# Optimization experiments

Measured on AMD Instinct MI355X. Metric: run time of the kernel, lower is better.

## Reference

```python
import jax, jax.numpy as jnp
import numpy as np

D_MODEL = 1024
NUM_HEADS = 16
D_HEAD = D_MODEL // NUM_HEADS


def rotate_half(x):
    half = x.shape[-1] // 2
    x1, x2 = x[..., :half], x[..., half:]
    return jnp.concatenate((-x2, x1), axis=-1)


def rope_cos_sin(seq_len, d_head, dtype):
    # inv_freq over even dims of d_head
    inv_freq = 1.0 / (10000.0 ** (jnp.arange(0, d_head, 2, dtype=jnp.float32) / d_head))
    t = jnp.arange(seq_len, dtype=jnp.float32)
    freqs = jnp.einsum('i,j->ij', t, inv_freq)        # [L, d_head/2]
    emb = jnp.concatenate((freqs, freqs), axis=-1)    # [L, d_head]
    return jnp.cos(emb).astype(dtype), jnp.sin(emb).astype(dtype)


def setup_inputs() -> dict:
    key = jax.random.key(0)
    ks = jax.random.split(key, 9)
    B, L = 2, 2048
    s = 1.0 / np.sqrt(D_MODEL)
    return {
        'x': jax.random.normal(ks[0], (B, L, D_MODEL), dtype=jnp.float32),
        'Wq': jax.random.normal(ks[1], (D_MODEL, D_MODEL), dtype=jnp.float32) * s,
        'bq': jax.random.normal(ks[2], (D_MODEL,), dtype=jnp.float32) * 0.02,
        'Wk': jax.random.normal(ks[3], (D_MODEL, D_MODEL), dtype=jnp.float32) * s,
        'bk': jax.random.normal(ks[4], (D_MODEL,), dtype=jnp.float32) * 0.02,
        'Wv': jax.random.normal(ks[5], (D_MODEL, D_MODEL), dtype=jnp.float32) * s,
        'bv': jax.random.normal(ks[6], (D_MODEL,), dtype=jnp.float32) * 0.02,
        'Wo': jax.random.normal(ks[7], (D_MODEL, D_MODEL), dtype=jnp.float32) * s,
        'bo': jax.random.normal(ks[8], (D_MODEL,), dtype=jnp.float32) * 0.02,
    }


def reference(x, Wq, bq, Wk, bk, Wv, bv, Wo, bo):
    B, L, D = x.shape
    H, Dh = NUM_HEADS, D_HEAD
    scale = Dh ** -0.5

    # projections: torch Linear is x @ W.T + b; here W stored as [in, out]-like
    # square matrices, so treat Wq etc. directly as x @ Wq + bq.
    q = (x @ Wq + bq).reshape(B, L, H, Dh).transpose(0, 2, 1, 3)  # [B,H,L,Dh]
    k = (x @ Wk + bk).reshape(B, L, H, Dh).transpose(0, 2, 1, 3)
    v = (x @ Wv + bv).reshape(B, L, H, Dh).transpose(0, 2, 1, 3)

    cos, sin = rope_cos_sin(L, Dh, x.dtype)  # [L, Dh]
    cos = cos[None, None]  # [1,1,L,Dh]
    sin = sin[None, None]
    q = q * cos + rotate_half(q) * sin
    k = k * cos + rotate_half(k) * sin

    attn = jnp.einsum('bhqd,bhkd->bhqk', q, k) * scale  # [B,H,L,L]
    attn = jax.nn.softmax(attn, axis=-1)
    out = jnp.einsum('bhqk,bhkd->bhqd', attn, v)        # [B,H,L,Dh]
    out = out.transpose(0, 2, 1, 3).reshape(B, L, D)
    return out @ Wo + bo
```

## Files before the change

### kernel.cpp

```cpp
#include <hip/hip_runtime.h>
#include <cmath>

#define D_MODEL  1024
#define NHEADS   16
#define DHEAD    64
#define BATCH    2
#define SEQ      2048
#define MROWS    (BATCH * SEQ)
#define HALF_DH  32
#define BHTOT    (BATCH * NHEADS)
#define QROWS    (BHTOT * SEQ)

typedef __attribute__((ext_vector_type(8))) short short8;
typedef __attribute__((ext_vector_type(4))) float f32x4;
typedef __attribute__((ext_vector_type(16))) float f32x16;

#define MFMA16(A,B,C) __builtin_amdgcn_mfma_f32_16x16x32_bf16(A,B,C,0,0,0)
#define MFMA32(A,B,C) __builtin_amdgcn_mfma_f32_32x32x16_bf16(A,B,C,0,0,0)

__device__ __forceinline__ unsigned short f2bf(float f) {
    unsigned int u = __float_as_uint(f);
    u += 0x7fffu + ((u >> 16) & 1u);
    return (unsigned short)(u >> 16);
}

__device__ __forceinline__ void gload_lds16(const void* g, void* l) {
    __builtin_amdgcn_global_load_lds(
        (const __attribute__((address_space(1))) unsigned int*)g,
        (__attribute__((address_space(3))) unsigned int*)l,
        16, 0, 0);
}

__global__ void rope_table_kernel(float* __restrict__ cosT, float* __restrict__ sinT) {
    int idx = blockIdx.x * blockDim.x + threadIdx.x;
    if (idx >= SEQ * HALF_DH) return;
    int l = idx >> 5;
    int j = idx & 31;
    float inv = powf(10000.0f, -(float)(2 * j) / (float)DHEAD);
    float ang = (float)l * inv;
    cosT[idx] = cosf(ang);
    sinT[idx] = sinf(ang);
}

__global__ __launch_bounds__(256)
void convert_bf16_kernel(const float* __restrict__ in, unsigned short* __restrict__ out) {
    int i = blockIdx.x * 256 + threadIdx.x;
    float4 v = ((const float4*)in)[i];
    ushort4 o;
    o.x = f2bf(v.x); o.y = f2bf(v.y); o.z = f2bf(v.z); o.w = f2bf(v.w);
    ((ushort4*)out)[i] = o;
}

__global__ __launch_bounds__(256)
void wtrans4_kernel(const float* __restrict__ Wq, const float* __restrict__ Wk,
                    const float* __restrict__ Wv, const float* __restrict__ Wo,
                    unsigned short* __restrict__ q, unsigned short* __restrict__ k,
                    unsigned short* __restrict__ v, unsigned short* __restrict__ o)
{
    __shared__ unsigned short T[64][68];
    const float* W; unsigned short* Wt;
    switch (blockIdx.z) {
        case 0:  W = Wq; Wt = q; break;
        case 1:  W = Wk; Wt = k; break;
        case 2:  W = Wv; Wt = v; break;
        default: W = Wo; Wt = o; break;
    }
    const int k0 = blockIdx.x * 64, n0 = blockIdx.y * 64;
    const int t = threadIdx.x, r = t >> 4, cq = t & 15;
    #pragma unroll
    for (int p = 0; p < 4; ++p) {
        int kk = r + 16 * p;
        float4 vv = *(const float4*)&W[(size_t)(k0 + kk) * D_MODEL + n0 + cq * 4];
        T[cq * 4 + 0][kk] = f2bf(vv.x);
        T[cq * 4 + 1][kk] = f2bf(vv.y);
        T[cq * 4 + 2][kk] = f2bf(vv.z);
        T[cq * 4 + 3][kk] = f2bf(vv.w);
    }
    __syncthreads();
    #pragma unroll
    for (int p = 0; p < 4; ++p) {
        int n = r + 16 * p;
        ushort4 ov;
        ov.x = T[n][cq * 4 + 0]; ov.y = T[n][cq * 4 + 1];
        ov.z = T[n][cq * 4 + 2]; ov.w = T[n][cq * 4 + 3];
        *(ushort4*)&Wt[(size_t)(n0 + n) * D_MODEL + k0 + cq * 4] = ov;
    }
}

__global__ __launch_bounds__(256)
void qkv_proj_kernel(const unsigned short* __restrict__ A,
                     const unsigned short* __restrict__ wqT, const unsigned short* __restrict__ wkT,
                     const unsigned short* __restrict__ wvT,
                     const float* __restrict__ bq, const float* __restrict__ bk,
                     const float* __restrict__ bv,
                     const float* __restrict__ cosT, const float* __restrict__ sinT,
                     unsigned short* __restrict__ qb, unsigned short* __restrict__ kb,
                     unsigned short* __restrict__ vtb)
{
    __shared__ unsigned short SMEM[128 * 64 + 64 * 64];
    unsigned short* As = SMEM;
    unsigned short* Bs = SMEM + 128 * 64;

    const int z = blockIdx.z;
    const unsigned short* Bt = (z == 0) ? wqT : (z == 1) ? wkT : wvT;
    const float* bias = (z == 0) ? bq : (z == 1) ? bk : bv;

    const int tid = threadIdx.x;
    const int w = tid >> 6, ln = tid & 63;
    const int c = ln & 15, g = ln >> 4;
    const int bm = blockIdx.x * 128, bn = blockIdx.y * 64;
    const int srow = ln >> 3, sblk = ln & 7;

    f32x4 acc[2][4];
    #pragma unroll
    for (int mi = 0; mi < 2; ++mi)
        #pragma unroll
        for (int ni = 0; ni < 4; ++ni) acc[mi][ni] = (f32x4){0.f, 0.f, 0.f, 0.f};

    for (int k0 = 0; k0 < D_MODEL; k0 += 64) {
        __syncthreads();
        #pragma unroll
        for (int i = 0; i < 4; ++i) {
            int chunk = w * 4 + i;
            int row = chunk * 8 + srow;
            int gcol = (sblk ^ (row & 7)) * 8;
            gload_lds16(&A[(size_t)(bm + row) * D_MODEL + k0 + gcol], &As[chunk * 512]);
        }
        #pragma unroll
        for (int i = 0; i < 2; ++i) {
            int chunk = w * 2 + i;
            int row = chunk * 8 + srow;
            int gcol = (sblk ^ (row & 7)) * 8;
            gload_lds16(&Bt[(size_t)(bn + row) * D_MODEL + k0 + gcol], &Bs[chunk * 512]);
        }
        __syncthreads();

        #pragma unroll
        for (int ks = 0; ks < 2; ++ks) {
            const int koff = (ks * 32 + g * 8) ^ ((c & 7) * 8);
            short8 af[2];
            #pragma unroll
            for (int mi = 0; mi < 2; ++mi)
                af[mi] = *(const short8*)&As[(w * 32 + mi * 16 + c) * 64 + koff];
            #pragma unroll
            for (int ni = 0; ni < 4; ++ni) {
                short8 bfr = *(const short8*)&Bs[(ni * 16 + c) * 64 + koff];
                #pragma unroll
                for (int mi = 0; mi < 2; ++mi)
                    acc[mi][ni] = MFMA16(af[mi], bfr, acc[mi][ni]);
            }
        }
    }

    float bv4[4];
    #pragma unroll
    for (int ni = 0; ni < 4; ++ni) bv4[ni] = bias[bn + ni * 16 + c];

    if (z < 2) {
        unsigned short* op = z ? kb : qb;
        const int hy = blockIdx.y;
        #pragma unroll
        for (int mi = 0; mi < 2; ++mi) {
            #pragma unroll
            for (int r = 0; r < 4; ++r) {
                const int m = bm + w * 32 + mi * 16 + g * 4 + r;
                const int b = m >> 11, ll = m & (SEQ - 1);
                float v[4];
                #pragma unroll
                for (int ni = 0; ni < 4; ++ni) v[ni] = acc[mi][ni][r] + bv4[ni];
                #pragma unroll
                for (int ni = 0; ni < 2; ++ni) {
                    int d = ni * 16 + c;
                    float co = cosT[ll * HALF_DH + d];
                    float si = sinT[ll * HALF_DH + d];
                    float lo = v[ni], hi = v[ni + 2];
                    v[ni]     = lo * co - hi * si;
                    v[ni + 2] = hi * co + lo * si;
                }
                unsigned short* dst = op + ((size_t)(b * NHEADS + hy) * SEQ + ll) * DHEAD;
                #pragma unroll
                for (int ni = 0; ni < 4; ++ni) dst[ni * 16 + c] = f2bf(v[ni]);
            }
        }
    } else {
        unsigned short (*T)[136] = (unsigned short(*)[136])SMEM;
        __syncthreads();
        #pragma unroll
        for (int mi = 0; mi < 2; ++mi)
            #pragma unroll
            for (int r = 0; r < 4; ++r)
                #pragma unroll
                for (int ni = 0; ni < 4; ++ni)
                    T[ni * 16 + c][w * 32 + mi * 16 + g * 4 + r] = f2bf(acc[mi][ni][r] + bv4[ni]);
        __syncthreads();
        const int b  = bm >> 11;
        const int l0 = bm & (SEQ - 1);
        const int bh = b * NHEADS + blockIdx.y;
        unsigned short* Vo = vtb + (size_t)bh * DHEAD * SEQ;
        #pragma unroll
        for (int it = 0; it < 4; ++it) {
            int row  = (tid >> 4) + it * 16;
            int col8 = tid & 15;
            uint4 val = *(const uint4*)&T[row][col8 * 8];
            *(uint4*)&Vo[(size_t)row * SEQ + l0 + col8 * 8] = val;
        }
    }
}

__global__ __launch_bounds__(256)
void outproj_kernel(const unsigned short* __restrict__ A, const unsigned short* __restrict__ Bt,
                    const float* __restrict__ bias, float* __restrict__ out)
{
    __shared__ unsigned short As[128 * 64];
    __shared__ unsigned short Bs[64 * 64];
    const int tid = threadIdx.x;
    const int w = tid >> 6, ln = tid & 63;
    const int c = ln & 15, g = ln >> 4;
    const int bm = blockIdx.x * 128, bn = blockIdx.y * 64;
    const int srow = ln >> 3, sblk = ln & 7;

    f32x4 acc[2][4];
    #pragma unroll
    for (int mi = 0; mi < 2; ++mi)
        #pragma unroll
        for (int ni = 0; ni < 4; ++ni) acc[mi][ni] = (f32x4){0.f, 0.f, 0.f, 0.f};

    for (int k0 = 0; k0 < D_MODEL; k0 += 64) {
        __syncthreads();
        #pragma unroll
        for (int i = 0; i < 4; ++i) {
            int chunk = w * 4 + i;
            int row = chunk * 8 + srow;
            int gcol = (sblk ^ (row & 7)) * 8;
            gload_lds16(&A[(size_t)(bm + row) * D_MODEL + k0 + gcol], &As[chunk * 512]);
        }
        #pragma unroll
        for (int i = 0; i < 2; ++i) {
            int chunk = w * 2 + i;
            int row = chunk * 8 + srow;
            int gcol = (sblk ^ (row & 7)) * 8;
            gload_lds16(&Bt[(size_t)(bn + row) * D_MODEL + k0 + gcol], &Bs[chunk * 512]);
        }
        __syncthreads();

        #pragma unroll
        for (int ks = 0; ks < 2; ++ks) {
            const int koff = (ks * 32 + g * 8) ^ ((c & 7) * 8);
            short8 af[2];
            #pragma unroll
            for (int mi = 0; mi < 2; ++mi)
                af[mi] = *(const short8*)&As[(w * 32 + mi * 16 + c) * 64 + koff];
            #pragma unroll
            for (int ni = 0; ni < 4; ++ni) {
                short8 bfr = *(const short8*)&Bs[(ni * 16 + c) * 64 + koff];
                #pragma unroll
                for (int mi = 0; mi < 2; ++mi)
                    acc[mi][ni] = MFMA16(af[mi], bfr, acc[mi][ni]);
            }
        }
    }

    float bv4[4];
    #pragma unroll
    for (int ni = 0; ni < 4; ++ni) bv4[ni] = bias[bn + ni * 16 + c];
    #pragma unroll
    for (int mi = 0; mi < 2; ++mi)
        #pragma unroll
        for (int r = 0; r < 4; ++r) {
            const int m = bm + w * 32 + mi * 16 + g * 4 + r;
            #pragma unroll
            for (int ni = 0; ni < 4; ++ni)
                out[(size_t)m * D_MODEL + bn + ni * 16 + c] = acc[mi][ni][r] + bv4[ni];
        }
}

__global__ __launch_bounds__(256, 4)
void attn_mfma32_kernel(const unsigned short* __restrict__ Q, const unsigned short* __restrict__ K,
                        const unsigned short* __restrict__ Vt, unsigned short* __restrict__ O,
                        float* __restrict__ accP, float* __restrict__ ml, int nsplit)
{
    __shared__ unsigned short Ks[2][64 * 64];
    __shared__ unsigned short Vs[2][64 * 64];
    const int tid = threadIdx.x;
    const int w = tid >> 6, ln = tid & 63;
    const int ql = ln & 31;
    const int h  = ln >> 5;
    const int bh = blockIdx.y;
    const int q  = blockIdx.x * 128 + w * 32 + ql;
    const int split = blockIdx.z;
    const int ntile = SEQ / (64 * nsplit);
    const int kt0 = split * (SEQ / nsplit);
    const float SC = 0.125f * 1.44269504088896340736f;
    const int srow = ln >> 3, sblk = ln & 7;

    const unsigned short* Qb = Q  + (size_t)bh * SEQ * DHEAD;
    const unsigned short* Kb = K  + (size_t)bh * SEQ * DHEAD;
    const unsigned short* Vb = Vt + (size_t)bh * DHEAD * SEQ;

    short8 qf[4];
    #pragma unroll
    for (int dk = 0; dk < 4; ++dk)
        qf[dk] = *(const short8*)&Qb[(size_t)q * DHEAD + dk * 16 + h * 8];

    f32x16 accO0, accO1;
    #pragma unroll
    for (int r = 0; r < 16; ++r) { accO0[r] = 0.f; accO1[r] = 0.f; }
    float accL = 0.f, mst = -1e30f;

    #pragma unroll
    for (int i = 0; i < 2; ++i) {
        int chunk = w * 2 + i;
        int row = chunk * 8 + srow;
        int gcol = (sblk ^ (row & 7)) * 8;
        gload_lds16(&Kb[(size_t)(kt0 + row) * DHEAD + gcol], &Ks[0][chunk * 512]);
        gload_lds16(&Vb[(size_t)row * SEQ + kt0 + gcol],     &Vs[0][chunk * 512]);
    }
    __syncthreads();

    int cur = 0;
    for (int it = 0; it < ntile; ++it) {
        const int kt = kt0 + it * 64;
        if (it + 1 < ntile) {
            #pragma unroll
            for (int i = 0; i < 2; ++i) {
                int chunk = w * 2 + i;
                int row = chunk * 8 + srow;
                int gcol = (sblk ^ (row & 7)) * 8;
                gload_lds16(&Kb[(size_t)(kt + 64 + row) * DHEAD + gcol], &Ks[cur ^ 1][chunk * 512]);
                gload_lds16(&Vb[(size_t)row * SEQ + kt + 64 + gcol],     &Vs[cur ^ 1][chunk * 512]);
            }
        }

        f32x16 s0, s1;
        #pragma unroll
        for (int r = 0; r < 16; ++r) { s0[r] = 0.f; s1[r] = 0.f; }
        #pragma unroll
        for (int dk = 0; dk < 4; ++dk) {
            const int off = ((2 * dk + h) ^ (ql & 7)) * 8;
            short8 kf0 = *(const short8*)&Ks[cur][ql * 64 + off];
            short8 kf1 = *(const short8*)&Ks[cur][(32 + ql) * 64 + off];
            s0 = MFMA32(kf0, qf[dk], s0);
            s1 = MFMA32(kf1, qf[dk], s1);
        }

        float m16[16];
        #pragma unroll
        for (int r = 0; r < 16; ++r) m16[r] = fmaxf(s0[r], s1[r]);
        #pragma unroll
        for (int st = 8; st >= 1; st >>= 1)
            #pragma unroll
            for (int r = 0; r < st; ++r) m16[r] = fmaxf(m16[r], m16[r + st]);
        float mx = m16[0];
        mx = fmaxf(mx, __shfl_xor(mx, 32));

        const float mn = fmaxf(mst, mx);
        if (__any(mn > mst)) {
            const float rsc = exp2f((mst - mn) * SC);
            #pragma unroll
            for (int r = 0; r < 16; ++r) { accO0[r] *= rsc; accO1[r] *= rsc; }
            accL *= rsc;
            mst = mn;
        }

        #pragma unroll
        for (int r = 0; r < 16; ++r) {
            s0[r] = exp2f((s0[r] - mst) * SC);
            s1[r] = exp2f((s1[r] - mst) * SC);
        }

        float t16[16];
        #pragma unroll
        for (int r = 0; r < 16; ++r) t16[r] = s0[r] + s1[r];
        #pragma unroll
        for (int st = 8; st >= 1; st >>= 1)
            #pragma unroll
            for (int r = 0; r < st; ++r) t16[r] += t16[r + st];
        float ts = t16[0];
        ts += __shfl_xor(ts, 32);
        accL += ts;

        short8 pf[4];
        #define REPACK_T(T, SV)                                                          \
        {                                                                                \
            unsigned int wA0, wA1, wB0, wB1;                                             \
            asm("v_cvt_pk_bf16_f32 %0, %1, %2" : "=v"(wA0)                               \
                : "v"((SV)[8 * ((T) & 1) + 0]), "v"((SV)[8 * ((T) & 1) + 1]));           \
            asm("v_cvt_pk_bf16_f32 %0, %1, %2" : "=v"(wA1)                               \
                : "v"((SV)[8 * ((T) & 1) + 2]), "v"((SV)[8 * ((T) & 1) + 3]));           \
            asm("v_cvt_pk_bf16_f32 %0, %1, %2" : "=v"(wB0)                               \
                : "v"((SV)[8 * ((T) & 1) + 4]), "v"((SV)[8 * ((T) & 1) + 5]));           \
            asm("v_cvt_pk_bf16_f32 %0, %1, %2" : "=v"(wB1)                               \
                : "v"((SV)[8 * ((T) & 1) + 6]), "v"((SV)[8 * ((T) & 1) + 7]));           \
            asm("v_permlane32_swap_b32 %0, %1" : "+v"(wA0), "+v"(wB0));                  \
            asm("v_permlane32_swap_b32 %0, %1" : "+v"(wA1), "+v"(wB1));                  \
            union { short8 v; unsigned int u[4]; } tmp;                                  \
            tmp.u[0] = wA0; tmp.u[1] = wA1; tmp.u[2] = wB0; tmp.u[3] = wB1;              \
            pf[T] = tmp.v;                                                               \
        }
        REPACK_T(0, s0) REPACK_T(1, s0) REPACK_T(2, s1) REPACK_T(3, s1)
        #undef REPACK_T

        #pragma unroll
        for (int t = 0; t < 4; ++t) {
            const int off = ((2 * t + h) ^ (ql & 7)) * 8;
            short8 vf0 = *(const short8*)&Vs[cur][ql * 64 + off];
            short8 vf1 = *(const short8*)&Vs[cur][(32 + ql) * 64 + off];
            accO0 = MFMA32(vf0, pf[t], accO0);
            accO1 = MFMA32(vf1, pf[t], accO1);
        }

        __syncthreads();
        cur ^= 1;
    }

    if (nsplit == 1) {
        const int b = bh >> 4, hh = bh & 15;
        const float inv = 1.0f / accL;
        unsigned short* dst = O + ((size_t)(b * SEQ + q)) * D_MODEL + hh * DHEAD;
        #define EPI(ACC, DC)                                                             \
        {                                                                                \
            _Pragma("unroll")                                                            \
            for (int rq = 0; rq < 4; ++rq) {                                             \
                float a0 = (ACC)[4 * rq + 0] * inv, a1 = (ACC)[4 * rq + 1] * inv;        \
                float a2 = (ACC)[4 * rq + 2] * inv, a3 = (ACC)[4 * rq + 3] * inv;        \
                unsigned int p0, p1;                                                     \
                asm("v_cvt_pk_bf16_f32 %0, %1, %2" : "=v"(p0) : "v"(a0), "v"(a1));       \
                asm("v_cvt_pk_bf16_f32 %0, %1, %2" : "=v"(p1) : "v"(a2), "v"(a3));       \
                uint2 pk; pk.x = p0; pk.y = p1;                                          \
                *(uint2*)(dst + 32 * (DC) + 8 * rq + 4 * h) = pk;                        \
            }                                                                            \
        }
        EPI(accO0, 0) EPI(accO1, 1)
        #undef EPI
    } else {
        float* base = accP + ((size_t)(split * BHTOT + bh) * SEQ + q) * 64;
        #pragma unroll
        for (int rq = 0; rq < 4; ++rq) {
            float4 v0, v1;
            v0.x = accO0[4 * rq + 0]; v0.y = accO0[4 * rq + 1];
            v0.z = accO0[4 * rq + 2]; v0.w = accO0[4 * rq + 3];
            v1.x = accO1[4 * rq + 0]; v1.y = accO1[4 * rq + 1];
            v1.z = accO1[4 * rq + 2]; v1.w = accO1[4 * rq + 3];
            *(float4*)&base[8 * rq + 4 * h]      = v0;
            *(float4*)&base[32 + 8 * rq + 4 * h] = v1;
        }
        if (h == 0) {
            float2 v; v.x = mst; v.y = accL;
            ((float2*)ml)[(size_t)(split * BHTOT + bh) * SEQ + q] = v;
        }
    }
}

__global__ __launch_bounds__(256)
void combine2_kernel(const float* __restrict__ accP, const float* __restrict__ ml,
                     unsigned short* __restrict__ ob)
{
    const float SC = 0.125f * 1.44269504088896340736f;
    int t = blockIdx.x * 256 + threadIdx.x;
    int d4  = (t & 15) * 4;
    int bhq = t >> 4;
    const float2* ML = (const float2*)ml;
    float2 m0 = ML[bhq];
    float2 m1 = ML[(size_t)QROWS + bhq];
    float M  = fmaxf(m0.x, m1.x);
    float w0 = exp2f((m0.x - M) * SC);
    float w1 = exp2f((m1.x - M) * SC);
    float inv = 1.0f / (w0 * m0.y + w1 * m1.y);
    float4 a0 = *(const float4*)&accP[(size_t)bhq * 64 + d4];
    float4 a1 = *(const float4*)&accP[(size_t)QROWS * 64 + (size_t)bhq * 64 + d4];
    float o0 = (a0.x * w0 + a1.x * w1) * inv;
    float o1 = (a0.y * w0 + a1.y * w1) * inv;
    float o2 = (a0.z * w0 + a1.z * w1) * inv;
    float o3 = (a0.w * w0 + a1.w * w1) * inv;
    int bh = bhq >> 11, q = bhq & (SEQ - 1);
    int b = bh >> 4, hh = bh & 15;
    ushort4 ov;
    ov.x = f2bf(o0); ov.y = f2bf(o1); ov.z = f2bf(o2); ov.w = f2bf(o3);
    *(ushort4*)&ob[((size_t)(b * SEQ + q)) * D_MODEL + hh * DHEAD + d4] = ov;
}

extern "C" void kernel_launch(void* const* d_in, const int* in_sizes, int n_in,
                              void* d_out, int out_size, void* d_ws, size_t ws_size,
                              hipStream_t stream)
{
    const float* x  = (const float*)d_in[0];
    const float* Wq = (const float*)d_in[1];
    const float* bq = (const float*)d_in[2];
    const float* Wk = (const float*)d_in[3];
    const float* bk = (const float*)d_in[4];
    const float* Wv = (const float*)d_in[5];
    const float* bv = (const float*)d_in[6];
    const float* Wo = (const float*)d_in[7];
    const float* bo = (const float*)d_in[8];

    char* p = (char*)d_ws;
    float* cosT = (float*)p;            p += (size_t)SEQ * HALF_DH * 4;
    float* sinT = (float*)p;            p += (size_t)SEQ * HALF_DH * 4;
    unsigned short* xb  = (unsigned short*)p; p += (size_t)MROWS * D_MODEL * 2;
    unsigned short* wqT = (unsigned short*)p; p += (size_t)D_MODEL * D_MODEL * 2;
    unsigned short* wkT = (unsigned short*)p; p += (size_t)D_MODEL * D_MODEL * 2;
    unsigned short* wvT = (unsigned short*)p; p += (size_t)D_MODEL * D_MODEL * 2;
    unsigned short* woT = (unsigned short*)p; p += (size_t)D_MODEL * D_MODEL * 2;
    unsigned short* qb  = (unsigned short*)p; p += (size_t)MROWS * D_MODEL * 2;
    unsigned short* kb  = (unsigned short*)p; p += (size_t)MROWS * D_MODEL * 2;
    unsigned short* vtb = (unsigned short*)p; p += (size_t)MROWS * D_MODEL * 2;
    unsigned short* ob  = (unsigned short*)p; p += (size_t)MROWS * D_MODEL * 2;
    float* accP = (float*)p;            p += (size_t)2 * QROWS * 64 * 4;
    float* ml   = (float*)p;            p += (size_t)2 * QROWS * 2 * 4;
    size_t need2 = (size_t)(p - (char*)d_ws);
    const int nsplit = (ws_size >= need2) ? 2 : 1;

    rope_table_kernel<<<(SEQ * HALF_DH + 255) / 256, 256, 0, stream>>>(cosT, sinT);
    convert_bf16_kernel<<<(MROWS * D_MODEL / 4) / 256, 256, 0, stream>>>(x, xb);

    wtrans4_kernel<<<dim3(D_MODEL / 64, D_MODEL / 64, 4), 256, 0, stream>>>(
        Wq, Wk, Wv, Wo, wqT, wkT, wvT, woT);

    qkv_proj_kernel<<<dim3(MROWS / 128, D_MODEL / 64, 3), 256, 0, stream>>>(
        xb, wqT, wkT, wvT, bq, bk, bv, cosT, sinT, qb, kb, vtb);

    attn_mfma32_kernel<<<dim3(SEQ / 128, BHTOT, nsplit), 256, 0, stream>>>(
        qb, kb, vtb, ob, accP, ml, nsplit);

    if (nsplit == 2)
        combine2_kernel<<<(QROWS * 16) / 256, 256, 0, stream>>>(accP, ml, ob);

    outproj_kernel<<<dim3(MROWS / 128, D_MODEL / 64), 256, 0, stream>>>(ob, woT, bo, (float*)d_out);
}
```

Measured before the change: 152.6 us.

## Enlarge GEMM M-tiles to 256 and compute softmax row sums via MFMA

```diff
diff --git a/kernel.cpp b/kernel.cpp
--- a/kernel.cpp
+++ b/kernel.cpp
@@ -97,9 +97,9 @@
                      unsigned short* __restrict__ qb, unsigned short* __restrict__ kb,
                      unsigned short* __restrict__ vtb)
 {
-    __shared__ unsigned short SMEM[128 * 64 + 64 * 64];
+    __shared__ unsigned short SMEM[256 * 64 + 64 * 64];
     unsigned short* As = SMEM;
-    unsigned short* Bs = SMEM + 128 * 64;
+    unsigned short* Bs = SMEM + 256 * 64;
 
     const int z = blockIdx.z;
     const unsigned short* Bt = (z == 0) ? wqT : (z == 1) ? wkT : wvT;
@@ -108,20 +108,20 @@
     const int tid = threadIdx.x;
     const int w = tid >> 6, ln = tid & 63;
     const int c = ln & 15, g = ln >> 4;
-    const int bm = blockIdx.x * 128, bn = blockIdx.y * 64;
+    const int bm = blockIdx.x * 256, bn = blockIdx.y * 64;
     const int srow = ln >> 3, sblk = ln & 7;
 
-    f32x4 acc[2][4];
-    #pragma unroll
-    for (int mi = 0; mi < 2; ++mi)
+    f32x4 acc[4][4];
+    #pragma unroll
+    for (int mi = 0; mi < 4; ++mi)
         #pragma unroll
         for (int ni = 0; ni < 4; ++ni) acc[mi][ni] = (f32x4){0.f, 0.f, 0.f, 0.f};
 
     for (int k0 = 0; k0 < D_MODEL; k0 += 64) {
         __syncthreads();
         #pragma unroll
-        for (int i = 0; i < 4; ++i) {
-            int chunk = w * 4 + i;
+        for (int i = 0; i < 8; ++i) {
+            int chunk = w * 8 + i;
             int row = chunk * 8 + srow;
             int gcol = (sblk ^ (row & 7)) * 8;
             gload_lds16(&A[(size_t)(bm + row) * D_MODEL + k0 + gcol], &As[chunk * 512]);
@@ -138,15 +138,15 @@
         #pragma unroll
         for (int ks = 0; ks < 2; ++ks) {
             const int koff = (ks * 32 + g * 8) ^ ((c & 7) * 8);
-            short8 af[2];
-            #pragma unroll
-            for (int mi = 0; mi < 2; ++mi)
-                af[mi] = *(const short8*)&As[(w * 32 + mi * 16 + c) * 64 + koff];
+            short8 af[4];
+            #pragma unroll
+            for (int mi = 0; mi < 4; ++mi)
+                af[mi] = *(const short8*)&As[(w * 64 + mi * 16 + c) * 64 + koff];
             #pragma unroll
             for (int ni = 0; ni < 4; ++ni) {
                 short8 bfr = *(const short8*)&Bs[(ni * 16 + c) * 64 + koff];
                 #pragma unroll
-                for (int mi = 0; mi < 2; ++mi)
+                for (int mi = 0; mi < 4; ++mi)
                     acc[mi][ni] = MFMA16(af[mi], bfr, acc[mi][ni]);
             }
         }
@@ -160,10 +160,10 @@
         unsigned short* op = z ? kb : qb;
         const int hy = blockIdx.y;
         #pragma unroll
-        for (int mi = 0; mi < 2; ++mi) {
+        for (int mi = 0; mi < 4; ++mi) {
             #pragma unroll
             for (int r = 0; r < 4; ++r) {
-                const int m = bm + w * 32 + mi * 16 + g * 4 + r;
+                const int m = bm + w * 64 + mi * 16 + g * 4 + r;
                 const int b = m >> 11, ll = m & (SEQ - 1);
                 float v[4];
                 #pragma unroll
@@ -183,26 +183,26 @@
             }
         }
     } else {
-        unsigned short (*T)[136] = (unsigned short(*)[136])SMEM;
-        __syncthreads();
-        #pragma unroll
-        for (int mi = 0; mi < 2; ++mi)
+        unsigned short (*T)[264] = (unsigned short(*)[264])SMEM;
+        __syncthreads();
+        #pragma unroll
+        for (int mi = 0; mi < 4; ++mi)
             #pragma unroll
             for (int r = 0; r < 4; ++r)
                 #pragma unroll
                 for (int ni = 0; ni < 4; ++ni)
-                    T[ni * 16 + c][w * 32 + mi * 16 + g * 4 + r] = f2bf(acc[mi][ni][r] + bv4[ni]);
+                    T[ni * 16 + c][w * 64 + mi * 16 + g * 4 + r] = f2bf(acc[mi][ni][r] + bv4[ni]);
         __syncthreads();
         const int b  = bm >> 11;
         const int l0 = bm & (SEQ - 1);
         const int bh = b * NHEADS + blockIdx.y;
         unsigned short* Vo = vtb + (size_t)bh * DHEAD * SEQ;
         #pragma unroll
-        for (int it = 0; it < 4; ++it) {
-            int row  = (tid >> 4) + it * 16;
-            int col8 = tid & 15;
-            uint4 val = *(const uint4*)&T[row][col8 * 8];
-            *(uint4*)&Vo[(size_t)row * SEQ + l0 + col8 * 8] = val;
+        for (int it = 0; it < 8; ++it) {
+            int row = (tid >> 5) + it * 8;
+            int ch  = tid & 31;
+            uint4 val = *(const uint4*)&T[row][ch * 8];
+            *(uint4*)&Vo[(size_t)row * SEQ + l0 + ch * 8] = val;
         }
     }
 }
@@ -211,25 +211,25 @@
 void outproj_kernel(const unsigned short* __restrict__ A, const unsigned short* __restrict__ Bt,
                     const float* __restrict__ bias, float* __restrict__ out)
 {
-    __shared__ unsigned short As[128 * 64];
+    __shared__ unsigned short As[256 * 64];
     __shared__ unsigned short Bs[64 * 64];
     const int tid = threadIdx.x;
     const int w = tid >> 6, ln = tid & 63;
     const int c = ln & 15, g = ln >> 4;
-    const int bm = blockIdx.x * 128, bn = blockIdx.y * 64;
+    const int bm = blockIdx.x * 256, bn = blockIdx.y * 64;
     const int srow = ln >> 3, sblk = ln & 7;
 
-    f32x4 acc[2][4];
-    #pragma unroll
-    for (int mi = 0; mi < 2; ++mi)
+    f32x4 acc[4][4];
+    #pragma unroll
+    for (int mi = 0; mi < 4; ++mi)
         #pragma unroll
         for (int ni = 0; ni < 4; ++ni) acc[mi][ni] = (f32x4){0.f, 0.f, 0.f, 0.f};
 
     for (int k0 = 0; k0 < D_MODEL; k0 += 64) {
         __syncthreads();
         #pragma unroll
-        for (int i = 0; i < 4; ++i) {
-            int chunk = w * 4 + i;
+        for (int i = 0; i < 8; ++i) {
+            int chunk = w * 8 + i;
             int row = chunk * 8 + srow;
             int gcol = (sblk ^ (row & 7)) * 8;
             gload_lds16(&A[(size_t)(bm + row) * D_MODEL + k0 + gcol], &As[chunk * 512]);
@@ -246,15 +246,15 @@
         #pragma unroll
         for (int ks = 0; ks < 2; ++ks) {
             const int koff = (ks * 32 + g * 8) ^ ((c & 7) * 8);
-            short8 af[2];
-            #pragma unroll
-            for (int mi = 0; mi < 2; ++mi)
-                af[mi] = *(const short8*)&As[(w * 32 + mi * 16 + c) * 64 + koff];
+            short8 af[4];
+            #pragma unroll
+            for (int mi = 0; mi < 4; ++mi)
+                af[mi] = *(const short8*)&As[(w * 64 + mi * 16 + c) * 64 + koff];
             #pragma unroll
             for (int ni = 0; ni < 4; ++ni) {
                 short8 bfr = *(const short8*)&Bs[(ni * 16 + c) * 64 + koff];
                 #pragma unroll
-                for (int mi = 0; mi < 2; ++mi)
+                for (int mi = 0; mi < 4; ++mi)
                     acc[mi][ni] = MFMA16(af[mi], bfr, acc[mi][ni]);
             }
         }
@@ -264,10 +264,10 @@
     #pragma unroll
     for (int ni = 0; ni < 4; ++ni) bv4[ni] = bias[bn + ni * 16 + c];
     #pragma unroll
-    for (int mi = 0; mi < 2; ++mi)
+    for (int mi = 0; mi < 4; ++mi)
         #pragma unroll
         for (int r = 0; r < 4; ++r) {
-            const int m = bm + w * 32 + mi * 16 + g * 4 + r;
+            const int m = bm + w * 64 + mi * 16 + g * 4 + r;
             #pragma unroll
             for (int ni = 0; ni < 4; ++ni)
                 out[(size_t)m * D_MODEL + bn + ni * 16 + c] = acc[mi][ni][r] + bv4[ni];
@@ -302,10 +302,19 @@
     for (int dk = 0; dk < 4; ++dk)
         qf[dk] = *(const short8*)&Qb[(size_t)q * DHEAD + dk * 16 + h * 8];
 
-    f32x16 accO0, accO1;
-    #pragma unroll
-    for (int r = 0; r < 16; ++r) { accO0[r] = 0.f; accO1[r] = 0.f; }
-    float accL = 0.f, mst = -1e30f;
+    short8 onesF;
+    #pragma unroll
+    for (int i = 0; i < 8; ++i) onesF[i] = (short)0x3F80;
+
+    int offk[4];
+    #pragma unroll
+    for (int t = 0; t < 4; ++t) offk[t] = ((2 * t + h) ^ (ql & 7)) * 8;
+    const int rA = ql * 64, rB = (32 + ql) * 64;
+
+    f32x16 accO0, accO1, accS;
+    #pragma unroll
+    for (int r = 0; r < 16; ++r) { accO0[r] = 0.f; accO1[r] = 0.f; accS[r] = 0.f; }
+    float mst = -1e30f;
 
     #pragma unroll
     for (int i = 0; i < 2; ++i) {
@@ -336,21 +345,28 @@
         for (int r = 0; r < 16; ++r) { s0[r] = 0.f; s1[r] = 0.f; }
         #pragma unroll
         for (int dk = 0; dk < 4; ++dk) {
-            const int off = ((2 * dk + h) ^ (ql & 7)) * 8;
-            short8 kf0 = *(const short8*)&Ks[cur][ql * 64 + off];
-            short8 kf1 = *(const short8*)&Ks[cur][(32 + ql) * 64 + off];
+            short8 kf0 = *(const short8*)&Ks[cur][rA + offk[dk]];
+            short8 kf1 = *(const short8*)&Ks[cur][rB + offk[dk]];
             s0 = MFMA32(kf0, qf[dk], s0);
             s1 = MFMA32(kf1, qf[dk], s1);
         }
 
-        float m16[16];
-        #pragma unroll
-        for (int r = 0; r < 16; ++r) m16[r] = fmaxf(s0[r], s1[r]);
-        #pragma unroll
-        for (int st = 8; st >= 1; st >>= 1)
-            #pragma unroll
-            for (int r = 0; r < st; ++r) m16[r] = fmaxf(m16[r], m16[r + st]);
-        float mx = m16[0];
+        float a0 = fmaxf(fmaxf(s0[0], s0[1]), s0[2]);
+        float a1 = fmaxf(fmaxf(s0[3], s0[4]), s0[5]);
+        float a2 = fmaxf(fmaxf(s0[6], s0[7]), s0[8]);
+        float a3 = fmaxf(fmaxf(s0[9], s0[10]), s0[11]);
+        float a4 = fmaxf(fmaxf(s0[12], s0[13]), s0[14]);
+        float a5 = fmaxf(fmaxf(s0[15], s1[0]), s1[1]);
+        float a6 = fmaxf(fmaxf(s1[2], s1[3]), s1[4]);
+        float a7 = fmaxf(fmaxf(s1[5], s1[6]), s1[7]);
+        float a8 = fmaxf(fmaxf(s1[8], s1[9]), s1[10]);
+        float a9 = fmaxf(fmaxf(s1[11], s1[12]), s1[13]);
+        float aA = fmaxf(s1[14], s1[15]);
+        float b0 = fmaxf(fmaxf(a0, a1), a2);
+        float b1 = fmaxf(fmaxf(a3, a4), a5);
+        float b2 = fmaxf(fmaxf(a6, a7), a8);
+        float b3 = fmaxf(a9, aA);
+        float mx = fmaxf(fmaxf(fmaxf(b0, b1), b2), b3);
         mx = fmaxf(mx, __shfl_xor(mx, 32));
 
         const float mn = fmaxf(mst, mx);
@@ -358,7 +374,7 @@
             const float rsc = exp2f((mst - mn) * SC);
             #pragma unroll
             for (int r = 0; r < 16; ++r) { accO0[r] *= rsc; accO1[r] *= rsc; }
-            accL *= rsc;
+            accS[0] *= rsc;
             mst = mn;
         }
 
@@ -367,17 +383,6 @@
             s0[r] = exp2f((s0[r] - mst) * SC);
             s1[r] = exp2f((s1[r] - mst) * SC);
         }
-
-        float t16[16];
-        #pragma unroll
-        for (int r = 0; r < 16; ++r) t16[r] = s0[r] + s1[r];
-        #pragma unroll
-        for (int st = 8; st >= 1; st >>= 1)
-            #pragma unroll
-            for (int r = 0; r < st; ++r) t16[r] += t16[r + st];
-        float ts = t16[0];
-        ts += __shfl_xor(ts, 32);
-        accL += ts;
 
         short8 pf[4];
         #define REPACK_T(T, SV)                                                          \
@@ -402,9 +407,9 @@
 
         #pragma unroll
         for (int t = 0; t < 4; ++t) {
-            const int off = ((2 * t + h) ^ (ql & 7)) * 8;
-            short8 vf0 = *(const short8*)&Vs[cur][ql * 64 + off];
-            short8 vf1 = *(const short8*)&Vs[cur][(32 + ql) * 64 + off];
+            short8 vf0 = *(const short8*)&Vs[cur][rA + offk[t]];
+            short8 vf1 = *(const short8*)&Vs[cur][rB + offk[t]];
+            accS  = MFMA32(onesF, pf[t], accS);
             accO0 = MFMA32(vf0, pf[t], accO0);
             accO1 = MFMA32(vf1, pf[t], accO1);
         }
@@ -413,6 +418,7 @@
         cur ^= 1;
     }
 
+    const float accL = accS[0];
     if (nsplit == 1) {
         const int b = bh >> 4, hh = bh & 15;
         const float inv = 1.0f / accL;
@@ -516,7 +522,7 @@
     wtrans4_kernel<<<dim3(D_MODEL / 64, D_MODEL / 64, 4), 256, 0, stream>>>(
         Wq, Wk, Wv, Wo, wqT, wkT, wvT, woT);
 
-    qkv_proj_kernel<<<dim3(MROWS / 128, D_MODEL / 64, 3), 256, 0, stream>>>(
+    qkv_proj_kernel<<<dim3(MROWS / 256, D_MODEL / 64, 3), 256, 0, stream>>>(
         xb, wqT, wkT, wvT, bq, bk, bv, cosT, sinT, qb, kb, vtb);
 
     attn_mfma32_kernel<<<dim3(SEQ / 128, BHTOT, nsplit), 256, 0, stream>>>(
@@ -525,5 +531,5 @@
     if (nsplit == 2)
         combine2_kernel<<<(QROWS * 16) / 256, 256, 0, stream>>>(accP, ml, ob);
 
-    outproj_kernel<<<dim3(MROWS / 128, D_MODEL / 64), 256, 0, stream>>>(ob, woT, bo, (float*)d_out);
-}
+    outproj_kernel<<<dim3(MROWS / 256, D_MODEL / 64), 256, 0, stream>>>(ob, woT, bo, (float*)d_out);
+}
```

Result: slower. 164.6 us (+7.9%).

## Merge prep kernels and compute softmax row sums via MFMA with ones

Applied to the files above, without the earlier changes.

```diff
diff --git a/kernel.cpp b/kernel.cpp
--- a/kernel.cpp
+++ b/kernel.cpp
@@ -31,59 +31,65 @@
         16, 0, 0);
 }
 
-__global__ void rope_table_kernel(float* __restrict__ cosT, float* __restrict__ sinT) {
-    int idx = blockIdx.x * blockDim.x + threadIdx.x;
-    if (idx >= SEQ * HALF_DH) return;
-    int l = idx >> 5;
-    int j = idx & 31;
-    float inv = powf(10000.0f, -(float)(2 * j) / (float)DHEAD);
-    float ang = (float)l * inv;
-    cosT[idx] = cosf(ang);
-    sinT[idx] = sinf(ang);
-}
-
 __global__ __launch_bounds__(256)
-void convert_bf16_kernel(const float* __restrict__ in, unsigned short* __restrict__ out) {
-    int i = blockIdx.x * 256 + threadIdx.x;
-    float4 v = ((const float4*)in)[i];
-    ushort4 o;
-    o.x = f2bf(v.x); o.y = f2bf(v.y); o.z = f2bf(v.z); o.w = f2bf(v.w);
-    ((ushort4*)out)[i] = o;
-}
-
-__global__ __launch_bounds__(256)
-void wtrans4_kernel(const float* __restrict__ Wq, const float* __restrict__ Wk,
-                    const float* __restrict__ Wv, const float* __restrict__ Wo,
-                    unsigned short* __restrict__ q, unsigned short* __restrict__ k,
-                    unsigned short* __restrict__ v, unsigned short* __restrict__ o)
+void prep_kernel(const float* __restrict__ x,
+                 const float* __restrict__ Wq, const float* __restrict__ Wk,
+                 const float* __restrict__ Wv, const float* __restrict__ Wo,
+                 unsigned short* __restrict__ xb,
+                 unsigned short* __restrict__ wqT, unsigned short* __restrict__ wkT,
+                 unsigned short* __restrict__ wvT, unsigned short* __restrict__ woT,
+                 float* __restrict__ cosT, float* __restrict__ sinT)
 {
     __shared__ unsigned short T[64][68];
-    const float* W; unsigned short* Wt;
-    switch (blockIdx.z) {
-        case 0:  W = Wq; Wt = q; break;
-        case 1:  W = Wk; Wt = k; break;
-        case 2:  W = Wv; Wt = v; break;
-        default: W = Wo; Wt = o; break;
-    }
-    const int k0 = blockIdx.x * 64, n0 = blockIdx.y * 64;
-    const int t = threadIdx.x, r = t >> 4, cq = t & 15;
-    #pragma unroll
-    for (int p = 0; p < 4; ++p) {
-        int kk = r + 16 * p;
-        float4 vv = *(const float4*)&W[(size_t)(k0 + kk) * D_MODEL + n0 + cq * 4];
-        T[cq * 4 + 0][kk] = f2bf(vv.x);
-        T[cq * 4 + 1][kk] = f2bf(vv.y);
-        T[cq * 4 + 2][kk] = f2bf(vv.z);
-        T[cq * 4 + 3][kk] = f2bf(vv.w);
-    }
-    __syncthreads();
-    #pragma unroll
-    for (int p = 0; p < 4; ++p) {
-        int n = r + 16 * p;
-        ushort4 ov;
-        ov.x = T[n][cq * 4 + 0]; ov.y = T[n][cq * 4 + 1];
-        ov.z = T[n][cq * 4 + 2]; ov.w = T[n][cq * 4 + 3];
-        *(ushort4*)&Wt[(size_t)(n0 + n) * D_MODEL + k0 + cq * 4] = ov;
+    const int bid = blockIdx.x;
+    const int tid = threadIdx.x;
+
+    if (bid < 4096) {
+        int i = bid * 256 + tid;
+        float4 v = ((const float4*)x)[i];
+        ushort4 o;
+        o.x = f2bf(v.x); o.y = f2bf(v.y); o.z = f2bf(v.z); o.w = f2bf(v.w);
+        ((ushort4*)xb)[i] = o;
+    } else if (bid < 5120) {
+        int b2 = bid - 4096;
+        int z  = b2 >> 8;
+        int bx = (b2 & 255) >> 4;
+        int by = b2 & 15;
+        const float* W; unsigned short* Wt;
+        switch (z) {
+            case 0:  W = Wq; Wt = wqT; break;
+            case 1:  W = Wk; Wt = wkT; break;
+            case 2:  W = Wv; Wt = wvT; break;
+            default: W = Wo; Wt = woT; break;
+        }
+        const int k0 = bx * 64, n0 = by * 64;
+        const int r = tid >> 4, cq = tid & 15;
+        #pragma unroll
+        for (int p = 0; p < 4; ++p) {
+            int kk = r + 16 * p;
+            float4 vv = *(const float4*)&W[(size_t)(k0 + kk) * D_MODEL + n0 + cq * 4];
+            T[cq * 4 + 0][kk] = f2bf(vv.x);
+            T[cq * 4 + 1][kk] = f2bf(vv.y);
+            T[cq * 4 + 2][kk] = f2bf(vv.z);
+            T[cq * 4 + 3][kk] = f2bf(vv.w);
+        }
+        __syncthreads();
+        #pragma unroll
+        for (int p = 0; p < 4; ++p) {
+            int n = r + 16 * p;
+            ushort4 ov;
+            ov.x = T[n][cq * 4 + 0]; ov.y = T[n][cq * 4 + 1];
+            ov.z = T[n][cq * 4 + 2]; ov.w = T[n][cq * 4 + 3];
+            *(ushort4*)&Wt[(size_t)(n0 + n) * D_MODEL + k0 + cq * 4] = ov;
+        }
+    } else {
+        int idx = (bid - 5120) * 256 + tid;
+        int l = idx >> 5;
+        int j = idx & 31;
+        float inv = powf(10000.0f, -(float)(2 * j) / (float)DHEAD);
+        float ang = (float)l * inv;
+        cosT[idx] = cosf(ang);
+        sinT[idx] = sinf(ang);
     }
 }
 
@@ -302,10 +308,19 @@
     for (int dk = 0; dk < 4; ++dk)
         qf[dk] = *(const short8*)&Qb[(size_t)q * DHEAD + dk * 16 + h * 8];
 
-    f32x16 accO0, accO1;
-    #pragma unroll
-    for (int r = 0; r < 16; ++r) { accO0[r] = 0.f; accO1[r] = 0.f; }
-    float accL = 0.f, mst = -1e30f;
+    short8 onesF;
+    #pragma unroll
+    for (int i = 0; i < 8; ++i) onesF[i] = (short)0x3F80;
+
+    int offk[4];
+    #pragma unroll
+    for (int t = 0; t < 4; ++t) offk[t] = ((2 * t + h) ^ (ql & 7)) * 8;
+    const int rA = ql * 64, rB = (32 + ql) * 64;
+
+    f32x16 accO0, accO1, accS;
+    #pragma unroll
+    for (int r = 0; r < 16; ++r) { accO0[r] = 0.f; accO1[r] = 0.f; accS[r] = 0.f; }
+    float mst = -1e30f;
 
     #pragma unroll
     for (int i = 0; i < 2; ++i) {
@@ -336,48 +351,42 @@
         for (int r = 0; r < 16; ++r) { s0[r] = 0.f; s1[r] = 0.f; }
         #pragma unroll
         for (int dk = 0; dk < 4; ++dk) {
-            const int off = ((2 * dk + h) ^ (ql & 7)) * 8;
-            short8 kf0 = *(const short8*)&Ks[cur][ql * 64 + off];
-            short8 kf1 = *(const short8*)&Ks[cur][(32 + ql) * 64 + off];
+            short8 kf0 = *(const short8*)&Ks[cur][rA + offk[dk]];
+            short8 kf1 = *(const short8*)&Ks[cur][rB + offk[dk]];
             s0 = MFMA32(kf0, qf[dk], s0);
             s1 = MFMA32(kf1, qf[dk], s1);
         }
 
-        float m16[16];
-        #pragma unroll
-        for (int r = 0; r < 16; ++r) m16[r] = fmaxf(s0[r], s1[r]);
-        #pragma unroll
-        for (int st = 8; st >= 1; st >>= 1)
-            #pragma unroll
-            for (int r = 0; r < st; ++r) m16[r] = fmaxf(m16[r], m16[r + st]);
-        float mx = m16[0];
+        float a0 = fmaxf(fmaxf(s0[0], s0[1]), s0[2]);
+        float a1 = fmaxf(fmaxf(s0[3], s0[4]), s0[5]);
+        float a2 = fmaxf(fmaxf(s0[6], s0[7]), s0[8]);
+        float a3 = fmaxf(fmaxf(s0[9], s0[10]), s0[11]);
+        float a4 = fmaxf(fmaxf(s0[12], s0[13]), s0[14]);
+        float a5 = fmaxf(fmaxf(s0[15], s1[0]), s1[1]);
+        float a6 = fmaxf(fmaxf(s1[2], s1[3]), s1[4]);
+        float a7 = fmaxf(fmaxf(s1[5], s1[6]), s1[7]);
+        float a8 = fmaxf(fmaxf(s1[8], s1[9]), s1[10]);
+        float a9 = fmaxf(fmaxf(s1[11], s1[12]), s1[13]);
+        float aA = fmaxf(s1[14], s1[15]);
+        float b0 = fmaxf(fmaxf(a0, a1), a2);
+        float b1 = fmaxf(fmaxf(a3, a4), a5);
+        float b2 = fmaxf(fmaxf(a6, a7), a8);
+        float b3 = fmaxf(a9, aA);
+        float mx = fmaxf(fmaxf(fmaxf(b0, b1), b2), b3);
         mx = fmaxf(mx, __shfl_xor(mx, 32));
 
         const float mn = fmaxf(mst, mx);
-        if (__any(mn > mst)) {
-            const float rsc = exp2f((mst - mn) * SC);
-            #pragma unroll
-            for (int r = 0; r < 16; ++r) { accO0[r] *= rsc; accO1[r] *= rsc; }
-            accL *= rsc;
-            mst = mn;
-        }
+        const float rsc = exp2f((mst - mn) * SC);
+        #pragma unroll
+        for (int r = 0; r < 16; ++r) { accO0[r] *= rsc; accO1[r] *= rsc; }
+        accS[0] *= rsc;
+        mst = mn;
 
         #pragma unroll
         for (int r = 0; r < 16; ++r) {
             s0[r] = exp2f((s0[r] - mst) * SC);
             s1[r] = exp2f((s1[r] - mst) * SC);
         }
-
-        float t16[16];
-        #pragma unroll
-        for (int r = 0; r < 16; ++r) t16[r] = s0[r] + s1[r];
-        #pragma unroll
-        for (int st = 8; st >= 1; st >>= 1)
-            #pragma unroll
-            for (int r = 0; r < st; ++r) t16[r] += t16[r + st];
-        float ts = t16[0];
-        ts += __shfl_xor(ts, 32);
-        accL += ts;
 
         short8 pf[4];
         #define REPACK_T(T, SV)                                                          \
@@ -402,9 +411,9 @@
 
         #pragma unroll
         for (int t = 0; t < 4; ++t) {
-            const int off = ((2 * t + h) ^ (ql & 7)) * 8;
-            short8 vf0 = *(const short8*)&Vs[cur][ql * 64 + off];
-            short8 vf1 = *(const short8*)&Vs[cur][(32 + ql) * 64 + off];
+            short8 vf0 = *(const short8*)&Vs[cur][rA + offk[t]];
+            short8 vf1 = *(const short8*)&Vs[cur][rB + offk[t]];
+            accS  = MFMA32(onesF, pf[t], accS);
             accO0 = MFMA32(vf0, pf[t], accO0);
             accO1 = MFMA32(vf1, pf[t], accO1);
         }
@@ -413,6 +422,7 @@
         cur ^= 1;
     }
 
+    const float accL = accS[0];
     if (nsplit == 1) {
         const int b = bh >> 4, hh = bh & 15;
         const float inv = 1.0f / accL;
@@ -510,11 +520,8 @@
     size_t need2 = (size_t)(p - (char*)d_ws);
     const int nsplit = (ws_size >= need2) ? 2 : 1;
 
-    rope_table_kernel<<<(SEQ * HALF_DH + 255) / 256, 256, 0, stream>>>(cosT, sinT);
-    convert_bf16_kernel<<<(MROWS * D_MODEL / 4) / 256, 256, 0, stream>>>(x, xb);
-
-    wtrans4_kernel<<<dim3(D_MODEL / 64, D_MODEL / 64, 4), 256, 0, stream>>>(
-        Wq, Wk, Wv, Wo, wqT, wkT, wvT, woT);
+    prep_kernel<<<5376, 256, 0, stream>>>(x, Wq, Wk, Wv, Wo,
+                                          xb, wqT, wkT, wvT, woT, cosT, sinT);
 
     qkv_proj_kernel<<<dim3(MROWS / 128, D_MODEL / 64, 3), 256, 0, stream>>>(
         xb, wqT, wkT, wvT, bq, bk, bv, cosT, sinT, qb, kb, vtb);
```

Result: no change. 151.9 us (-0.4%).
